# Optimization experiments

Hardware: AMD Instinct MI355X
Metric: run time of the kernel (lower is better)

Reference implementation:

```python
import jax, jax.numpy as jnp
import numpy as np

N_NODES = 50000
N_EDGES = 800000
FT = 128
HID = 128
N_EXTRA_LAYERS = 2  # num_layers - 1


def _gin_conv(x, src, dst, W1, b1, W2, b2):
    # GINConv with eps=0: mlp(x + sum_{j->i} x_j)
    agg = jax.ops.segment_sum(x[src], dst, num_segments=N_NODES)
    h = x + agg
    h = jax.nn.relu(h @ W1 + b1)
    return h @ W2 + b2


def setup_inputs() -> dict:
    key = jax.random.key(0)
    ks = jax.random.split(key, 12)
    feat = jax.random.normal(ks[0], (N_NODES, FT), dtype=jnp.float32)
    edge_index = jax.random.randint(ks[1], (2, N_EDGES), 0, N_NODES, dtype=jnp.int32)
    s = 0.02
    # layer 0: ft -> hid
    W1a = jax.random.normal(ks[2], (FT, HID), dtype=jnp.float32) * s
    b1a = jnp.zeros((HID,), dtype=jnp.float32)
    W2a = jax.random.normal(ks[3], (HID, HID), dtype=jnp.float32) * s
    b2a = jnp.zeros((HID,), dtype=jnp.float32)
    # remaining layers stacked: [L, hid, hid]
    Ws1 = jax.random.normal(ks[4], (N_EXTRA_LAYERS, HID, HID), dtype=jnp.float32) * s
    bs1 = jnp.zeros((N_EXTRA_LAYERS, HID), dtype=jnp.float32)
    Ws2 = jax.random.normal(ks[5], (N_EXTRA_LAYERS, HID, HID), dtype=jnp.float32) * s
    bs2 = jnp.zeros((N_EXTRA_LAYERS, HID), dtype=jnp.float32)
    return {"feat": feat, "edge_index": edge_index,
            "W1a": W1a, "b1a": b1a, "W2a": W2a, "b2a": b2a,
            "Ws1": Ws1, "bs1": bs1, "Ws2": Ws2, "bs2": bs2}


def reference(feat, edge_index, W1a, b1a, W2a, b2a, Ws1, bs1, Ws2, bs2):
    src = edge_index[0]
    dst = edge_index[1]
    x = jax.nn.relu(_gin_conv(feat, src, dst, W1a, b1a, W2a, b2a))
    for i in range(N_EXTRA_LAYERS):
        x = jax.nn.relu(_gin_conv(x, src, dst, Ws1[i], bs1[i], Ws2[i], bs2[i]))
    return x[None]  # [1, N, hid]
```

## Files before the change

### kernel.cpp

```cpp
#include <hip/hip_runtime.h>
#include <hip/hip_bf16.h>

#define N_NODES 50000
#define N_EDGES 800000
#define HID 128

typedef __attribute__((ext_vector_type(8))) short bf16x8;
typedef __attribute__((ext_vector_type(4))) float f32x4;

__device__ inline ushort f32_to_bf16_bits(float v) {
    union { float f; unsigned u; } a; a.f = v;
    unsigned r = a.u + 0x7fff + ((a.u >> 16) & 1);
    return (ushort)(r >> 16);
}
__device__ inline float bf16bits_to_f32(ushort b) {
    union { float f; unsigned u; } a; a.u = ((unsigned)b) << 16;
    return a.f;
}


__global__ __launch_bounds__(256) void prologue_kernel(const float* __restrict__ feat,
                                                       const int* __restrict__ dst,
                                                       const float* __restrict__ W1a,
                                                       const float* __restrict__ W2a,
                                                       const float* __restrict__ Ws1,
                                                       const float* __restrict__ Ws2,
                                                       ushort* __restrict__ xbA,
                                                       short* __restrict__ whi,
                                                       short* __restrict__ wlo,
                                                       int* __restrict__ cnt) {
    const int gtid = blockIdx.x * 256 + threadIdx.x;
    const int GS = 262144;

    for (int t = gtid; t < 800000; t += GS) {
        const float4* in4 = (const float4*)feat;
        float4 a = in4[2 * t], b = in4[2 * t + 1];
        float v[8] = {a.x, a.y, a.z, a.w, b.x, b.y, b.z, b.w};
        uint4 o;
        o.x = (unsigned)f32_to_bf16_bits(v[0]) | ((unsigned)f32_to_bf16_bits(v[1]) << 16);
        o.y = (unsigned)f32_to_bf16_bits(v[2]) | ((unsigned)f32_to_bf16_bits(v[3]) << 16);
        o.z = (unsigned)f32_to_bf16_bits(v[4]) | ((unsigned)f32_to_bf16_bits(v[5]) << 16);
        o.w = (unsigned)f32_to_bf16_bits(v[6]) | ((unsigned)f32_to_bf16_bits(v[7]) << 16);
        ((uint4*)xbA)[t] = o;
    }

    if (gtid < 6 * 2048) {
        int mat = gtid >> 11;
        int tid2 = gtid & 2047;
        const float* W;
        switch (mat) {
            case 0: W = W1a; break;
            case 1: W = W2a; break;
            case 2: W = Ws1; break;
            case 3: W = Ws2; break;
            case 4: W = Ws1 + HID * HID; break;
            default: W = Ws2 + HID * HID; break;
        }
        int l = tid2 & 63;
        int ft = tid2 >> 6;
        int t = ft & 3, f = ft >> 2;
        int g = l >> 4, lm = l & 15;
        bf16x8 hv, lv;
        #pragma unroll
        for (int i = 0; i < 8; ++i) {
            int k = t * 32 + g * 8 + i;
            int n = f * 16 + lm;
            float v = W[k * HID + n];
            ushort hb = f32_to_bf16_bits(v);
            ushort lb = f32_to_bf16_bits(v - bf16bits_to_f32(hb));
            hv[i] = (short)hb;
            lv[i] = (short)lb;
        }
        size_t base = ((size_t)mat * 2048 + tid2) * 8;
        *(bf16x8*)&whi[base] = hv;
        *(bf16x8*)&wlo[base] = lv;
    }

    for (int e = gtid; e < N_EDGES; e += GS) {
        atomicAdd(&cnt[dst[e]], 1);
    }
}


__global__ __launch_bounds__(256) void alloc_offsets_kernel(const int* __restrict__ cnt,
                                                            int* __restrict__ offs,
                                                            int* __restrict__ cursor,
                                                            int* __restrict__ gcur) {
    int i = blockIdx.x * 256 + threadIdx.x;
    int lane = threadIdx.x & 63;
    int c = (i < N_NODES) ? cnt[i] : 0;
    int pre = c;
    #pragma unroll
    for (int d = 1; d < 64; d <<= 1) {
        int t = __shfl_up(pre, d);
        if (lane >= d) pre += t;
    }
    int base = 0;
    if (lane == 63) base = atomicAdd(gcur, pre);
    base = __shfl(base, 63);
    int o = base + pre - c;
    if (i < N_NODES) { offs[i] = o; cursor[i] = o; }
}


__global__ __launch_bounds__(256) void scatter_kernel(const int* __restrict__ src,
                                                      const int* __restrict__ dst,
                                                      int* __restrict__ cursor,
                                                      ushort* __restrict__ csr16) {
    int e0 = blockIdx.x * 512 + threadIdx.x;
    int e1 = e0 + 256;
    int d0 = (e0 < N_EDGES) ? dst[e0] : 0;
    int d1 = (e1 < N_EDGES) ? dst[e1] : 0;
    int s0 = (e0 < N_EDGES) ? src[e0] : 0;
    int s1 = (e1 < N_EDGES) ? src[e1] : 0;
    if (e0 < N_EDGES) {
        int p0 = atomicAdd(&cursor[d0], 1);
        __builtin_nontemporal_store((ushort)s0, &csr16[p0]);
    }
    if (e1 < N_EDGES) {
        int p1 = atomicAdd(&cursor[d1], 1);
        __builtin_nontemporal_store((ushort)s1, &csr16[p1]);
    }
}


__global__ __launch_bounds__(256) void fused_gin_kernel(const unsigned* __restrict__ xbf,
                                                        const ushort* __restrict__ csr16,
                                                        const int* __restrict__ offs,
                                                        const int* __restrict__ cnt,
                                                        const short* __restrict__ w1hi,
                                                        const short* __restrict__ w1lo,
                                                        const short* __restrict__ w2hi,
                                                        const short* __restrict__ w2lo,
                                                        const float* __restrict__ b1,
                                                        const float* __restrict__ b2,
                                                        ushort* __restrict__ xoutb,
                                                        float* __restrict__ xoutf) {
    __shared__ short sHi[16][136];
    __shared__ short sLo[16][136];

    const int tid = threadIdx.x;
    const int lane = tid & 63;
    const int wid = tid >> 6;
    const int nbase = blockIdx.x * 16;
    const int g = lane >> 4, lm = lane & 15;

    for (int n = 0; n < 4; ++n) {
        int node = nbase + wid * 4 + n;
        int off = offs[node];
        int c = cnt[node];
        unsigned su = xbf[(size_t)node * 64 + lane];
        float ax = __uint_as_float(su << 16);
        float ay = __uint_as_float(su & 0xffff0000u);
        int e = 0;
        for (; e + 16 <= c; e += 16) {
            int s[16];
            #pragma unroll
            for (int q = 0; q < 16; ++q) s[q] = csr16[off + e + q];
            unsigned u[16];
            #pragma unroll
            for (int q = 0; q < 16; ++q) u[q] = xbf[(size_t)s[q] * 64 + lane];
            #pragma unroll
            for (int q = 0; q < 16; ++q) {
                ax += __uint_as_float(u[q] << 16);
                ay += __uint_as_float(u[q] & 0xffff0000u);
            }
        }
        for (; e + 4 <= c; e += 4) {
            int s0 = csr16[off + e], s1 = csr16[off + e + 1];
            int s2 = csr16[off + e + 2], s3 = csr16[off + e + 3];
            unsigned u0 = xbf[(size_t)s0 * 64 + lane];
            unsigned u1 = xbf[(size_t)s1 * 64 + lane];
            unsigned u2 = xbf[(size_t)s2 * 64 + lane];
            unsigned u3 = xbf[(size_t)s3 * 64 + lane];
            ax += (__uint_as_float(u0 << 16) + __uint_as_float(u1 << 16)) +
                  (__uint_as_float(u2 << 16) + __uint_as_float(u3 << 16));
            ay += (__uint_as_float(u0 & 0xffff0000u) + __uint_as_float(u1 & 0xffff0000u)) +
                  (__uint_as_float(u2 & 0xffff0000u) + __uint_as_float(u3 & 0xffff0000u));
        }
        for (; e < c; ++e) {
            int s = csr16[off + e];
            unsigned u = xbf[(size_t)s * 64 + lane];
            ax += __uint_as_float(u << 16);
            ay += __uint_as_float(u & 0xffff0000u);
        }
        ushort hx = f32_to_bf16_bits(ax);
        ushort lx = f32_to_bf16_bits(ax - bf16bits_to_f32(hx));
        ushort hy = f32_to_bf16_bits(ay);
        ushort ly = f32_to_bf16_bits(ay - bf16bits_to_f32(hy));
        int row = wid * 4 + n;
        *(unsigned*)&sHi[row][2 * lane] = (unsigned)hx | ((unsigned)hy << 16);
        *(unsigned*)&sLo[row][2 * lane] = (unsigned)lx | ((unsigned)ly << 16);
    }
    __syncthreads();

    f32x4 accT[2];

    {
        bf16x8 ahi[4], alo[4];
        #pragma unroll
        for (int t = 0; t < 4; ++t) {
            ahi[t] = *(bf16x8*)&sHi[lm][t * 32 + g * 8];
            alo[t] = *(bf16x8*)&sLo[lm][t * 32 + g * 8];
        }
        __syncthreads();
        #pragma unroll
        for (int ff = 0; ff < 2; ++ff) {
            int f = wid * 2 + ff;
            const bf16x8* bh = (const bf16x8*)&w1hi[((size_t)(f * 4) * 64 + lane) * 8];
            const bf16x8* bl = (const bf16x8*)&w1lo[((size_t)(f * 4) * 64 + lane) * 8];
            f32x4 acc = {0.f, 0.f, 0.f, 0.f};
            #pragma unroll
            for (int t = 0; t < 4; ++t) {
                bf16x8 bhv = bh[t * 64];
                bf16x8 blv = bl[t * 64];
                acc = __builtin_amdgcn_mfma_f32_16x16x32_bf16(ahi[t], bhv, acc, 0, 0, 0);
                acc = __builtin_amdgcn_mfma_f32_16x16x32_bf16(alo[t], bhv, acc, 0, 0, 0);
                acc = __builtin_amdgcn_mfma_f32_16x16x32_bf16(ahi[t], blv, acc, 0, 0, 0);
            }
            accT[ff] = acc;
        }
    }
    #pragma unroll
    for (int ff = 0; ff < 2; ++ff) {
        int f = wid * 2 + ff;
        float bv = b1[f * 16 + lm];
        #pragma unroll
        for (int r = 0; r < 4; ++r) {
            float v = accT[ff][r] + bv;
            v = v > 0.f ? v : 0.f;
            ushort hb = f32_to_bf16_bits(v);
            ushort lb = f32_to_bf16_bits(v - bf16bits_to_f32(hb));
            int m = g * 4 + r;
            sHi[m][f * 16 + lm] = (short)hb;
            sLo[m][f * 16 + lm] = (short)lb;
        }
    }
    __syncthreads();

    {
        bf16x8 ahi[4], alo[4];
        #pragma unroll
        for (int t = 0; t < 4; ++t) {
            ahi[t] = *(bf16x8*)&sHi[lm][t * 32 + g * 8];
            alo[t] = *(bf16x8*)&sLo[lm][t * 32 + g * 8];
        }
        #pragma unroll
        for (int ff = 0; ff < 2; ++ff) {
            int f = wid * 2 + ff;
            const bf16x8* bh = (const bf16x8*)&w2hi[((size_t)(f * 4) * 64 + lane) * 8];
            const bf16x8* bl = (const bf16x8*)&w2lo[((size_t)(f * 4) * 64 + lane) * 8];
            f32x4 acc = {0.f, 0.f, 0.f, 0.f};
            #pragma unroll
            for (int t = 0; t < 4; ++t) {
                bf16x8 bhv = bh[t * 64];
                bf16x8 blv = bl[t * 64];
                acc = __builtin_amdgcn_mfma_f32_16x16x32_bf16(ahi[t], bhv, acc, 0, 0, 0);
                acc = __builtin_amdgcn_mfma_f32_16x16x32_bf16(alo[t], bhv, acc, 0, 0, 0);
                acc = __builtin_amdgcn_mfma_f32_16x16x32_bf16(ahi[t], blv, acc, 0, 0, 0);
            }
            accT[ff] = acc;
        }
    }
    #pragma unroll
    for (int ff = 0; ff < 2; ++ff) {
        int f = wid * 2 + ff;
        float bv = b2[f * 16 + lm];
        #pragma unroll
        for (int r = 0; r < 4; ++r) {
            float v = accT[ff][r] + bv;
            v = v > 0.f ? v : 0.f;
            int gn = nbase + g * 4 + r;
            size_t gi = (size_t)gn * HID + f * 16 + lm;
            if (xoutb) xoutb[gi] = f32_to_bf16_bits(v);
            if (xoutf) xoutf[gi] = v;
        }
    }
}


extern "C" void kernel_launch(void* const* d_in, const int* in_sizes, int n_in,
                              void* d_out, int out_size, void* d_ws, size_t ws_size,
                              hipStream_t stream) {
    const float* feat = (const float*)d_in[0];
    const int* edge = (const int*)d_in[1];
    const int* src = edge;
    const int* dst = edge + N_EDGES;
    const float* W1a = (const float*)d_in[2];
    const float* b1a = (const float*)d_in[3];
    const float* W2a = (const float*)d_in[4];
    const float* b2a = (const float*)d_in[5];
    const float* Ws1 = (const float*)d_in[6];
    const float* bs1 = (const float*)d_in[7];
    const float* Ws2 = (const float*)d_in[8];
    const float* bs2 = (const float*)d_in[9];
    float* out = (float*)d_out;

    int* cnt = (int*)d_ws;
    int* gcur = cnt + 50176;
    int* offs = gcur + 64;
    int* cursor = offs + 50176;
    ushort* csr16 = (ushort*)(cursor + 50176);
    ushort* xbA = csr16 + N_EDGES;
    ushort* xbB = xbA + (size_t)N_NODES * HID;
    short* whi = (short*)(xbB + (size_t)N_NODES * HID);
    short* wlo = whi + 6 * 2048 * 8;

    hipMemsetAsync(cnt, 0, (50176 + 64) * sizeof(int), stream);

    prologue_kernel<<<1024, 256, 0, stream>>>(feat, dst, W1a, W2a, Ws1, Ws2,
                                              xbA, whi, wlo, cnt);
    alloc_offsets_kernel<<<(N_NODES + 255) / 256, 256, 0, stream>>>(cnt, offs, cursor, gcur);
    scatter_kernel<<<(N_EDGES + 511) / 512, 256, 0, stream>>>(src, dst, cursor, csr16);

    const int FB = N_NODES / 16;
    const int MS = 16384;

    fused_gin_kernel<<<FB, 256, 0, stream>>>((const unsigned*)xbA, csr16, offs, cnt,
                                             whi + 0 * MS, wlo + 0 * MS,
                                             whi + 1 * MS, wlo + 1 * MS, b1a, b2a,
                                             xbB, nullptr);
    fused_gin_kernel<<<FB, 256, 0, stream>>>((const unsigned*)xbB, csr16, offs, cnt,
                                             whi + 2 * MS, wlo + 2 * MS,
                                             whi + 3 * MS, wlo + 3 * MS, bs1, bs2,
                                             xbA, nullptr);
    fused_gin_kernel<<<FB, 256, 0, stream>>>((const unsigned*)xbA, csr16, offs, cnt,
                                             whi + 4 * MS, wlo + 4 * MS,
                                             whi + 5 * MS, wlo + 5 * MS,
                                             bs1 + HID, bs2 + HID,
                                             nullptr, out);
}
```

Measured before the change: 337.6 us.

## Build CSR via two-pass bucket partition by destination group before scatter

Replaces the single-pass random atomic scatter into CSR with two passes. The first partitions edges into 64-node destination buckets using per-bucket cursors and packed staging words. The second scatters within buckets so the per-node atomics and 16-bit writes land in localized regions. This aims to cut scattered atomic and write traffic, at the cost of an extra kernel launch plus a staging buffer write and read. Packing dst into the upper 16 bits would truncate node ids above 65535, which is safe here since N_NODES is 50000.

```diff
diff --git a/kernel.cpp b/kernel.cpp
--- a/kernel.cpp
+++ b/kernel.cpp
@@ -85,7 +85,8 @@
 __global__ __launch_bounds__(256) void alloc_offsets_kernel(const int* __restrict__ cnt,
                                                             int* __restrict__ offs,
                                                             int* __restrict__ cursor,
-                                                            int* __restrict__ gcur) {
+                                                            int* __restrict__ gcur,
+                                                            int* __restrict__ bcur) {
     int i = blockIdx.x * 256 + threadIdx.x;
     int lane = threadIdx.x & 63;
     int c = (i < N_NODES) ? cnt[i] : 0;
@@ -99,27 +100,38 @@
     if (lane == 63) base = atomicAdd(gcur, pre);
     base = __shfl(base, 63);
     int o = base + pre - c;
-    if (i < N_NODES) { offs[i] = o; cursor[i] = o; }
-}
-
-
-__global__ __launch_bounds__(256) void scatter_kernel(const int* __restrict__ src,
-                                                      const int* __restrict__ dst,
-                                                      int* __restrict__ cursor,
-                                                      ushort* __restrict__ csr16) {
-    int e0 = blockIdx.x * 512 + threadIdx.x;
-    int e1 = e0 + 256;
-    int d0 = (e0 < N_EDGES) ? dst[e0] : 0;
-    int d1 = (e1 < N_EDGES) ? dst[e1] : 0;
-    int s0 = (e0 < N_EDGES) ? src[e0] : 0;
-    int s1 = (e1 < N_EDGES) ? src[e1] : 0;
-    if (e0 < N_EDGES) {
-        int p0 = atomicAdd(&cursor[d0], 1);
-        __builtin_nontemporal_store((ushort)s0, &csr16[p0]);
-    }
-    if (e1 < N_EDGES) {
-        int p1 = atomicAdd(&cursor[d1], 1);
-        __builtin_nontemporal_store((ushort)s1, &csr16[p1]);
+    if (i < N_NODES) {
+        offs[i] = o;
+        cursor[i] = o;
+        if (lane == 0) bcur[i >> 6] = o;
+    }
+}
+
+
+__global__ __launch_bounds__(256) void partition_kernel(const int* __restrict__ src,
+                                                        const int* __restrict__ dst,
+                                                        int* __restrict__ bcur,
+                                                        unsigned* __restrict__ staging) {
+    int e = blockIdx.x * 256 + threadIdx.x;
+    if (e < N_EDGES) {
+        int d = dst[e];
+        int s = src[e];
+        int p = atomicAdd(&bcur[d >> 6], 1);
+        staging[p] = (unsigned)s | ((unsigned)d << 16);
+    }
+}
+
+
+__global__ __launch_bounds__(256) void scatter2_kernel(const unsigned* __restrict__ staging,
+                                                       int* __restrict__ cursor,
+                                                       ushort* __restrict__ csr16) {
+    int p = blockIdx.x * 256 + threadIdx.x;
+    if (p < N_EDGES) {
+        unsigned v = staging[p];
+        int s = v & 0xffff;
+        int d = v >> 16;
+        int pos = atomicAdd(&cursor[d], 1);
+        csr16[pos] = (ushort)s;
     }
 }
 
@@ -298,10 +310,12 @@
 
     int* cnt = (int*)d_ws;
     int* gcur = cnt + 50176;
-    int* offs = gcur + 64;
+    int* bcur = gcur + 64;
+    int* offs = bcur + 784;
     int* cursor = offs + 50176;
     ushort* csr16 = (ushort*)(cursor + 50176);
-    ushort* xbA = csr16 + N_EDGES;
+    unsigned* staging = (unsigned*)(csr16 + N_EDGES);
+    ushort* xbA = (ushort*)(staging + N_EDGES);
     ushort* xbB = xbA + (size_t)N_NODES * HID;
     short* whi = (short*)(xbB + (size_t)N_NODES * HID);
     short* wlo = whi + 6 * 2048 * 8;
@@ -310,8 +324,10 @@
 
     prologue_kernel<<<1024, 256, 0, stream>>>(feat, dst, W1a, W2a, Ws1, Ws2,
                                               xbA, whi, wlo, cnt);
-    alloc_offsets_kernel<<<(N_NODES + 255) / 256, 256, 0, stream>>>(cnt, offs, cursor, gcur);
-    scatter_kernel<<<(N_EDGES + 511) / 512, 256, 0, stream>>>(src, dst, cursor, csr16);
+    alloc_offsets_kernel<<<(N_NODES + 255) / 256, 256, 0, stream>>>(cnt, offs, cursor,
+                                                                    gcur, bcur);
+    partition_kernel<<<(N_EDGES + 255) / 256, 256, 0, stream>>>(src, dst, bcur, staging);
+    scatter2_kernel<<<(N_EDGES + 255) / 256, 256, 0, stream>>>(staging, cursor, csr16);
 
     const int FB = N_NODES / 16;
     const int MS = 16384;
```

New measurement: 515.0 us. +52.5%, slower.
